# Kernel optimization log

Measured on AMD Instinct MI355X. Metric: run time of the kernel, lower is better.

Reference implementation:

```python
import jax, jax.numpy as jnp
import numpy as np
import math

CH = 512
HEADS = 8
GROUPS = 32
EPS = 1e-5


def group_norm(x, w, b):
    # x: [B, C, T]
    B, C, T = x.shape
    xg = x.reshape(B, GROUPS, C // GROUPS, T)
    mu = xg.mean(axis=(2, 3), keepdims=True)
    var = xg.var(axis=(2, 3), keepdims=True)
    xg = (xg - mu) * jax.lax.rsqrt(var + EPS)
    return xg.reshape(B, C, T) * w[None, :, None] + b[None, :, None]


def conv1x1(x, w, b):
    # x: [B, C, T], w: [O, C, 1]
    return jnp.einsum('oc,bct->bot', w[:, :, 0], x) + b[None, :, None]


def conv3_same(x, w, b):
    y = jax.lax.conv_general_dilated(x, w, window_strides=(1,), padding='SAME',
                                     dimension_numbers=('NCH', 'OIH', 'NCH'))
    return y + b[None, :, None]


def setup_inputs() -> dict:
    key = jax.random.key(0)
    ks = jax.random.split(key, 12)
    B, Ti, Ts = 2, 4096, 1024
    inp = {
        'image': jax.random.normal(ks[0], (B, Ti, CH), jnp.float32),
        'st': jax.random.normal(ks[1], (B, Ts, CH), jnp.float32),
        'xn_w': jnp.ones((CH,), jnp.float32),
        'xn_b': jnp.zeros((CH,), jnp.float32),
        'jn_w': jnp.ones((CH,), jnp.float32),
        'jn_b': jnp.zeros((CH,), jnp.float32),
        'xqkv_w': jax.random.normal(ks[2], (3 * CH, CH, 1), jnp.float32) * (1.0 / math.sqrt(CH)),
        'xqkv_b': jnp.zeros((3 * CH,), jnp.float32),
        'jqkv_w': jax.random.normal(ks[3], (3 * CH, CH, 1), jnp.float32) * (1.0 / math.sqrt(CH)),
        'jqkv_b': jnp.zeros((3 * CH,), jnp.float32),
        # NOTE: original zero-inits proj; we use small random weights so the
        # attention path contributes to the output (same math).
        'proj_w': jax.random.normal(ks[4], (CH, CH, 3), jnp.float32) * (0.02 / math.sqrt(3 * CH)),
        'proj_b': jnp.zeros((CH,), jnp.float32),
    }
    return inp


def reference(image, st, xn_w, xn_b, jn_w, jn_b, xqkv_w, xqkv_b, jqkv_w, jqkv_b, proj_w, proj_b):
    # image: [B, Ti, C]  st: [B, Ts, C]
    x = image.transpose(0, 2, 1)           # [B, C, Ti]
    jc = st.transpose(0, 2, 1)              # [B, C, Ts]

    x_qkv = conv1x1(group_norm(x, xn_w, xn_b), xqkv_w, xqkv_b)    # [B, 3C, Ti]
    jc_qkv = conv1x1(group_norm(jc, jn_w, jn_b), jqkv_w, jqkv_b)  # [B, 3C, Ts]

    B, _, Ti = x_qkv.shape
    ch = CH // HEADS
    scale = 1.0 / math.sqrt(math.sqrt(ch))

    img_q = x_qkv[:, :CH].reshape(B, HEADS, ch, Ti)
    st_k = jc_qkv[:, CH:2 * CH].reshape(B, HEADS, ch, -1)
    st_v = jc_qkv[:, 2 * CH:].reshape(B, HEADS, ch, -1)

    # cross-attention: image queries attend to st keys/values
    w = jnp.einsum('bhct,bhcs->bhts', img_q * scale, st_k * scale)  # [B,H,Ti,Ts]
    w = jax.nn.softmax(w.astype(jnp.float32), axis=-1).astype(w.dtype)
    attn = jnp.einsum('bhts,bhcs->bhct', w, st_v).reshape(B, CH, Ti)

    x_h = conv3_same(attn, proj_w, proj_b)
    return x + x_h  # [B, C, Ti]
```

## Files before the change

kernel.cpp:

```cpp
#include <hip/hip_runtime.h>
#include <math.h>

static constexpr int CH = 512;
static constexpr int GROUPS = 32;
static constexpr int HC = 64;
static constexpr float EPS = 1e-5f;
static constexpr int TI = 4096;
static constexpr int TS = 1024;

typedef __bf16 bf16x8 __attribute__((ext_vector_type(8)));
typedef __bf16 bf16x4 __attribute__((ext_vector_type(4)));
typedef float f32x4 __attribute__((ext_vector_type(4)));

__global__ __launch_bounds__(256) void k_gn_stats(const float* __restrict__ X, int T,
                                                  float* __restrict__ stats) {
  int b = blockIdx.x >> 5;
  int g = blockIdx.x & 31;
  int tid = threadIdx.x;
  const float* base = X + ((size_t)b * T) * CH + g * 16;
  double s1 = 0.0, s2 = 0.0;
  for (int t = tid; t < T; t += 256) {
    const float4* p = (const float4*)(base + (size_t)t * CH);
#pragma unroll
    for (int q = 0; q < 4; ++q) {
      float4 v = p[q];
      s1 += (double)v.x + (double)v.y + (double)v.z + (double)v.w;
      s2 += (double)v.x * v.x + (double)v.y * v.y + (double)v.z * v.z + (double)v.w * v.w;
    }
  }
  __shared__ double r1[256];
  __shared__ double r2[256];
  r1[tid] = s1;
  r2[tid] = s2;
  __syncthreads();
  for (int s = 128; s > 0; s >>= 1) {
    if (tid < s) { r1[tid] += r1[tid + s]; r2[tid] += r2[tid + s]; }
    __syncthreads();
  }
  if (tid == 0) {
    double N = (double)16 * T;
    double mu = r1[0] / N;
    double var = r2[0] / N - mu * mu;
    float rs = (float)(1.0 / sqrt(var + (double)EPS));
    stats[(b * GROUPS + g) * 2 + 0] = (float)mu;
    stats[(b * GROUPS + g) * 2 + 1] = rs;
  }
}

__global__ __launch_bounds__(256) void k_gn_apply(const float* __restrict__ X,
                                                  const float* __restrict__ stats,
                                                  const float* __restrict__ nw,
                                                  const float* __restrict__ nb,
                                                  __bf16* __restrict__ Xp, int T) {
  size_t idx = ((size_t)blockIdx.x * 256 + threadIdx.x) * 8;
  int b = (int)(idx / ((size_t)T * 512));
  size_t rem = idx - (size_t)b * T * 512;
  int t = (int)(rem >> 9);
  int c = (int)(rem & 511);
  int g = c >> 4;
  float mu = stats[(b * GROUPS + g) * 2 + 0];
  float rs = stats[(b * GROUPS + g) * 2 + 1];
  float4 v0 = *(const float4*)(X + idx);
  float4 v1 = *(const float4*)(X + idx + 4);
  float4 w0 = *(const float4*)(nw + c);
  float4 w1 = *(const float4*)(nw + c + 4);
  float4 q0 = *(const float4*)(nb + c);
  float4 q1 = *(const float4*)(nb + c + 4);
  float xv[8] = {v0.x, v0.y, v0.z, v0.w, v1.x, v1.y, v1.z, v1.w};
  float wv[8] = {w0.x, w0.y, w0.z, w0.w, w1.x, w1.y, w1.z, w1.w};
  float qv[8] = {q0.x, q0.y, q0.z, q0.w, q1.x, q1.y, q1.z, q1.w};
  bf16x8 r;
#pragma unroll
  for (int i = 0; i < 8; ++i) {
    float a = rs * wv[i];
    r[i] = (__bf16)fmaf(xv[i], a, qv[i] - mu * a);
  }
  size_t off = ((((size_t)b * (T >> 4) + (t >> 4)) * 16 + (c >> 5)) * 64 +
                ((c >> 3) & 3) * 16 + (t & 15)) * 8;
  *(bf16x8*)(Xp + off) = r;
}

__global__ __launch_bounds__(256) void k_wpack(const float* __restrict__ W,
                                               __bf16* __restrict__ Wp) {
  int idx = blockIdx.x * 256 + threadIdx.x;
  int lane = idx & 63;
  int l = lane & 15, g = lane >> 4;
  int cb = (idx >> 6) & 15;
  int ob = idx >> 10;
  const float* src = W + (size_t)(ob * 16 + l) * 512 + cb * 32 + g * 8;
  float4 v0 = *(const float4*)src;
  float4 v1 = *(const float4*)(src + 4);
  float xv[8] = {v0.x, v0.y, v0.z, v0.w, v1.x, v1.y, v1.z, v1.w};
  bf16x8 r;
#pragma unroll
  for (int i = 0; i < 8; ++i) r[i] = (__bf16)xv[i];
  *(bf16x8*)(Wp + (size_t)idx * 8) = r;
}

__global__ __launch_bounds__(256) void k_wpack3(const float* __restrict__ W,
                                                __bf16* __restrict__ W3p) {
  int idx = blockIdx.x * 256 + threadIdx.x;
  int lane = idx & 63;
  int l = lane & 15, g = lane >> 4;
  int ob = (idx >> 6) & 31;
  int q = idx >> 11;
  int tap = q % 3;
  int cb = q / 3;
  int o = ob * 16 + l;
  int c = cb * 32 + g * 8;
  bf16x8 r;
#pragma unroll
  for (int j = 0; j < 8; ++j) r[j] = (__bf16)W[((size_t)o * 512 + c + j) * 3 + tap];
  *(bf16x8*)(W3p + (size_t)idx * 8) = r;
}

__global__ __launch_bounds__(256) void k_qkv_mfma(const __bf16* __restrict__ Xp,
                                                  const __bf16* __restrict__ Wp,
                                                  const float* __restrict__ bias,
                                                  __bf16* __restrict__ outQK,
                                                  __bf16* __restrict__ outVp,
                                                  int T) {
  int b = blockIdx.z;
  int o0 = blockIdx.y * 64;
  int tid = threadIdx.x;
  int w = tid >> 6;
  int lane = tid & 63;
  int l = lane & 15;
  int g = lane >> 4;
  int t0 = blockIdx.x * 128 + w * 32;
  int Tb = T >> 4;
  bool vmode = (outVp != nullptr) && (o0 >= 512);

  __shared__ __align__(16) __bf16 Elds[4][2048];

  f32x4 acc[2][4] = {};
  const __bf16* Xb = Xp + (size_t)b * T * 512;

  auto load_c = [&](int cb, bf16x8 (&af)[2], bf16x8 (&wf)[4]) {
#pragma unroll
    for (int m = 0; m < 2; ++m)
      af[m] = *(const bf16x8*)(Xb + ((((size_t)(t0 >> 4) + m) * 16 + cb) * 64 + lane) * 8);
#pragma unroll
    for (int n = 0; n < 4; ++n)
      wf[n] = *(const bf16x8*)(Wp + ((((size_t)(o0 >> 4) + n) * 16 + cb) * 64 + lane) * 8);
  };

  bf16x8 afA[2], wfA[4], afB[2], wfB[4];
#define QKV_LOOP(MMEXPR)                                                        \
  {                                                                             \
    load_c(0, afA, wfA);                                                        \
    _Pragma("unroll") for (int cb = 0; cb < 16; cb += 2) {                      \
      load_c(cb + 1, afB, wfB);                                                 \
      _Pragma("unroll") for (int m = 0; m < 2; ++m)                             \
          _Pragma("unroll") for (int n = 0; n < 4; ++n) {                       \
        bf16x8 af = afA[m], wf = wfA[n];                                        \
        acc[m][n] = MMEXPR;                                                     \
      }                                                                         \
      if (cb + 2 < 16) load_c(cb + 2, afA, wfA);                                \
      _Pragma("unroll") for (int m = 0; m < 2; ++m)                             \
          _Pragma("unroll") for (int n = 0; n < 4; ++n) {                       \
        bf16x8 af = afB[m], wf = wfB[n];                                        \
        acc[m][n] = MMEXPR;                                                     \
      }                                                                         \
    }                                                                           \
  }

  if (!vmode) {
    QKV_LOOP(__builtin_amdgcn_mfma_f32_16x16x32_bf16(wf, af, acc[m][n], 0, 0, 0))
    float sc = (outVp == nullptr) ? 0.125f : 1.0f;
    int swz = (l & 7) << 1;
    __bf16(*Eq)[64] = reinterpret_cast<__bf16(*)[64]>(&Elds[w][0]);
#pragma unroll
    for (int m = 0; m < 2; ++m)
#pragma unroll
      for (int n = 0; n < 4; ++n) {
        f32x4 bv = *(const f32x4*)(bias + o0 + 16 * n + 4 * g);
        bf16x4 pv;
#pragma unroll
        for (int r = 0; r < 4; ++r) pv[r] = (__bf16)((acc[m][n][r] + bv[r]) * sc);
        *(bf16x4*)&Eq[m * 16 + l][((4 * n + g) ^ swz) * 4] = pv;
      }
#pragma unroll
    for (int m = 0; m < 2; ++m)
#pragma unroll
      for (int cbi = 0; cbi < 2; ++cbi) {
        bf16x8 v = *(const bf16x8*)&Eq[m * 16 + l][((8 * cbi + 2 * g) ^ swz) * 4];
        *(bf16x8*)(outQK +
                   ((((size_t)b * Tb + (t0 >> 4) + m) * 16 + (o0 >> 5) + cbi) * 64 + lane) * 8) = v;
      }
  } else {
    QKV_LOOP(__builtin_amdgcn_mfma_f32_16x16x32_bf16(af, wf, acc[m][n], 0, 0, 0))
    int swzv = l & 6;
    __bf16(*Ev)[32] = reinterpret_cast<__bf16(*)[32]>(&Elds[w][0]);
#pragma unroll
    for (int m = 0; m < 2; ++m)
#pragma unroll
      for (int n = 0; n < 4; ++n) {
        float bo = bias[o0 + 16 * n + l];
        bf16x4 pv;
#pragma unroll
        for (int r = 0; r < 4; ++r) pv[r] = (__bf16)(acc[m][n][r] + bo);
        *(bf16x4*)&Ev[16 * n + l][((4 * m + g) ^ swzv) * 4] = pv;
      }
#pragma unroll
    for (int n = 0; n < 4; ++n) {
      bf16x8 v = *(const bf16x8*)&Ev[16 * n + l][((2 * g) ^ swzv) * 4];
      int cb16 = ((o0 - 512) >> 4) + n;
      *(bf16x8*)(outVp + ((((size_t)b * 32 + cb16) * 32 + (t0 >> 5)) * 64 + lane) * 8) = v;
    }
  }
#undef QKV_LOOP
}

__global__ __launch_bounds__(128, 4) void k_attn_mfma(const __bf16* __restrict__ Qp,
                                                      const __bf16* __restrict__ Kp,
                                                      const __bf16* __restrict__ Vp,
                                                      __bf16* __restrict__ outA) {
  int b = blockIdx.z;
  int h = blockIdx.y;
  int tid = threadIdx.x;
  int w = tid >> 6;
  int lane = tid & 63;
  int l = lane & 15;
  int g = lane >> 4;
  int t0 = blockIdx.x * 32;
  int swz = (l & 7) << 1;

  __shared__ __align__(16) __bf16 Pt[2][2][16][64];
  __shared__ float Ored[64][32];
  __shared__ float Lred[64][2];

  bf16x8 qf[2][2];
#pragma unroll
  for (int m = 0; m < 2; ++m)
#pragma unroll
    for (int ks = 0; ks < 2; ++ks)
      qf[m][ks] = *(const bf16x8*)(Qp + ((((size_t)b * 256 + (t0 >> 4) + m) * 16 +
                                          2 * h + ks) * 64 + lane) * 8);

  f32x4 o_acc[2][4] = {};
  float rs_acc[2] = {};

  int s_base = w * 512;
#pragma unroll 1
  for (int s0 = s_base; s0 < s_base + 512; s0 += 64) {
    bf16x8 kf[4][2];
#pragma unroll
    for (int n = 0; n < 4; ++n)
#pragma unroll
      for (int ks = 0; ks < 2; ++ks)
        kf[n][ks] = *(const bf16x8*)(Kp + ((((size_t)b * 64 + (s0 >> 4) + n) * 16 +
                                            2 * h + ks) * 64 + lane) * 8);
    bf16x8 vf[4][2];
#pragma unroll
    for (int n = 0; n < 4; ++n)
#pragma unroll
      for (int ks = 0; ks < 2; ++ks)
        vf[n][ks] = *(const bf16x8*)(Vp + ((((size_t)b * 32 + h * 4 + n) * 32 +
                                            (s0 >> 5) + ks) * 64 + lane) * 8);
    f32x4 sT[4][2];
#pragma unroll
    for (int sb = 0; sb < 4; ++sb)
#pragma unroll
      for (int tb = 0; tb < 2; ++tb) {
        f32x4 z = {0.f, 0.f, 0.f, 0.f};
        z = __builtin_amdgcn_mfma_f32_16x16x32_bf16(kf[sb][0], qf[tb][0], z, 0, 0, 0);
        sT[sb][tb] = __builtin_amdgcn_mfma_f32_16x16x32_bf16(kf[sb][1], qf[tb][1], z, 0, 0, 0);
      }
#pragma unroll
    for (int tb = 0; tb < 2; ++tb)
#pragma unroll
      for (int sb = 0; sb < 4; ++sb) {
        float p0 = __expf(sT[sb][tb][0]);
        float p1 = __expf(sT[sb][tb][1]);
        float p2 = __expf(sT[sb][tb][2]);
        float p3 = __expf(sT[sb][tb][3]);
        rs_acc[tb] += (p0 + p1) + (p2 + p3);
        bf16x4 pv;
        pv[0] = (__bf16)p0;
        pv[1] = (__bf16)p1;
        pv[2] = (__bf16)p2;
        pv[3] = (__bf16)p3;
        *(bf16x4*)&Pt[w][tb][l][((4 * sb + g) ^ swz) * 4] = pv;
      }
    bf16x8 pa[2][2];
#pragma unroll
    for (int tb = 0; tb < 2; ++tb)
#pragma unroll
      for (int ks = 0; ks < 2; ++ks)
        pa[tb][ks] = *(const bf16x8*)&Pt[w][tb][l][((8 * ks + 2 * g) ^ swz) * 4];
#pragma unroll
    for (int tb = 0; tb < 2; ++tb)
#pragma unroll
      for (int n = 0; n < 4; ++n) {
        o_acc[tb][n] = __builtin_amdgcn_mfma_f32_16x16x32_bf16(vf[n][0], pa[tb][0], o_acc[tb][n], 0, 0, 0);
        o_acc[tb][n] = __builtin_amdgcn_mfma_f32_16x16x32_bf16(vf[n][1], pa[tb][1], o_acc[tb][n], 0, 0, 0);
      }
  }

  if (w == 1) {
#pragma unroll
    for (int tb = 0; tb < 2; ++tb) {
#pragma unroll
      for (int n = 0; n < 4; ++n)
#pragma unroll
        for (int r = 0; r < 4; ++r) Ored[lane][tb * 16 + n * 4 + r] = o_acc[tb][n][r];
      Lred[lane][tb] = rs_acc[tb];
    }
  }
  __syncthreads();
  if (w == 0) {
#pragma unroll
    for (int tb = 0; tb < 2; ++tb) {
#pragma unroll
      for (int n = 0; n < 4; ++n)
#pragma unroll
        for (int r = 0; r < 4; ++r) o_acc[tb][n][r] += Ored[lane][tb * 16 + n * 4 + r];
      float v = rs_acc[tb] + Lred[lane][tb];
      v += __shfl_xor(v, 16, 64);
      v += __shfl_xor(v, 32, 64);
      float inv = 1.f / v;
#pragma unroll
      for (int n = 0; n < 4; ++n) {
        bf16x4 ov;
#pragma unroll
        for (int r = 0; r < 4; ++r) ov[r] = (__bf16)(o_acc[tb][n][r] * inv);
        *(bf16x4*)(outA + ((size_t)b * TI + t0 + 16 * tb + l) * 512 + h * 64 + 16 * n + 4 * g) = ov;
      }
    }
  }
}

__global__ __launch_bounds__(256) void k_conv3_mfma(const __bf16* __restrict__ A,
                                                    const __bf16* __restrict__ W3p,
                                                    const float* __restrict__ bias,
                                                    const float* __restrict__ image,
                                                    float* __restrict__ out) {
  int b = blockIdx.z;
  int o0 = blockIdx.y * 64;
  int ob0 = o0 >> 4;
  int tid = threadIdx.x;
  int w = tid >> 6;
  int lane = tid & 63;
  int l = lane & 15;
  int g = lane >> 4;
  int t0 = blockIdx.x * 128;
  int t0w = t0 + w * 32;

  __shared__ __align__(16) __bf16 Alds[2][130 * 32];
  __shared__ __align__(16) __bf16 Wlds[2][12 * 512];

  const __bf16* Ab = A + (size_t)b * TI * 512;

  auto stage = [&](int cb, int buf) {
#pragma unroll
    for (int pass = 0; pass < 3; ++pass) {
      int gi = tid + pass * 256;
      if (gi < 520) {
        int r = gi >> 2, gg = gi & 3;
        int t = t0 - 1 + r;
        bf16x8 v = {};
        if (t >= 0 && t < TI) v = *(const bf16x8*)(Ab + (size_t)t * 512 + cb * 32 + gg * 8);
        *(bf16x8*)&Alds[buf][r * 32 + ((gg ^ (r & 3)) << 3)] = v;
      }
    }
#pragma unroll
    for (int ch = w; ch < 12; ch += 4) {
      bf16x8 v = *(const bf16x8*)(W3p + ((((size_t)cb * 3 + (ch >> 2)) * 32 + ob0 +
                                          (ch & 3)) * 64 + lane) * 8);
      *(bf16x8*)&Wlds[buf][ch * 512 + lane * 8] = v;
    }
  };

  f32x4 acc[2][4] = {};

  stage(0, 0);
  __syncthreads();
#pragma unroll 1
  for (int cs = 0; cs < 16; ++cs) {
    int cur = cs & 1;
    if (cs < 15) stage(cs + 1, cur ^ 1);
    bf16x8 af[3][2], wf[3][4];
#pragma unroll
    for (int tap = 0; tap < 3; ++tap) {
#pragma unroll
      for (int m = 0; m < 2; ++m) {
        int r = w * 32 + 16 * m + l + tap;
        af[tap][m] = *(const bf16x8*)&Alds[cur][r * 32 + ((g ^ (r & 3)) << 3)];
      }
#pragma unroll
      for (int n = 0; n < 4; ++n)
        wf[tap][n] = *(const bf16x8*)&Wlds[cur][(tap * 4 + n) * 512 + lane * 8];
    }
#pragma unroll
    for (int tap = 0; tap < 3; ++tap)
#pragma unroll
      for (int m = 0; m < 2; ++m)
#pragma unroll
        for (int n = 0; n < 4; ++n)
          acc[m][n] =
              __builtin_amdgcn_mfma_f32_16x16x32_bf16(af[tap][m], wf[tap][n], acc[m][n], 0, 0, 0);
    __syncthreads();
  }

#pragma unroll
  for (int m = 0; m < 2; ++m) {
    int tb = t0w + 16 * m + 4 * g;
#pragma unroll
    for (int n = 0; n < 4; ++n) {
      int o = o0 + 16 * n + l;
      float bo = bias[o];
      f32x4 r;
#pragma unroll
      for (int rr = 0; rr < 4; ++rr)
        r[rr] = acc[m][n][rr] + bo + image[((size_t)b * TI + tb + rr) * CH + o];
      *(f32x4*)(out + ((size_t)b * CH + o) * TI + tb) = r;
    }
  }
}

extern "C" void kernel_launch(void* const* d_in, const int* in_sizes, int n_in,
                              void* d_out, int out_size, void* d_ws, size_t ws_size,
                              hipStream_t stream) {
  const float* image = (const float*)d_in[0];
  const float* st = (const float*)d_in[1];
  const float* xn_w = (const float*)d_in[2];
  const float* xn_b = (const float*)d_in[3];
  const float* jn_w = (const float*)d_in[4];
  const float* jn_b = (const float*)d_in[5];
  const float* xqkv_w = (const float*)d_in[6];
  const float* xqkv_b = (const float*)d_in[7];
  const float* jqkv_w = (const float*)d_in[8];
  const float* jqkv_b = (const float*)d_in[9];
  const float* proj_w = (const float*)d_in[10];
  const float* proj_b = (const float*)d_in[11];
  float* out = (float*)d_out;
  float* ws = (float*)d_ws;

  float* stats_x = ws;
  float* stats_j = ws + 128;
  __bf16* Xnp = (__bf16*)(ws + 256);
  __bf16* abuf = Xnp;
  __bf16* stnp = Xnp + (size_t)2 * TI * CH;
  __bf16* wqb = stnp + (size_t)2 * TS * CH;
  __bf16* wkvb = wqb + (size_t)CH * CH;
  __bf16* wb3 = wkvb + (size_t)2 * CH * CH;
  __bf16* Qp = wb3 + (size_t)3 * CH * CH;
  __bf16* Kp = Qp + (size_t)2 * TI * CH;
  __bf16* Vp = Kp + (size_t)2 * TS * CH;

  k_gn_stats<<<dim3(64), dim3(256), 0, stream>>>(image, TI, stats_x);
  k_gn_stats<<<dim3(64), dim3(256), 0, stream>>>(st, TS, stats_j);

  k_gn_apply<<<dim3(2 * TI * 512 / 2048), dim3(256), 0, stream>>>(image, stats_x, xn_w, xn_b, Xnp, TI);
  k_gn_apply<<<dim3(2 * TS * 512 / 2048), dim3(256), 0, stream>>>(st, stats_j, jn_w, jn_b, stnp, TS);

  k_wpack<<<dim3(128), dim3(256), 0, stream>>>(xqkv_w, wqb);
  k_wpack<<<dim3(256), dim3(256), 0, stream>>>(jqkv_w + (size_t)CH * CH, wkvb);
  k_wpack3<<<dim3(384), dim3(256), 0, stream>>>(proj_w, wb3);

  k_qkv_mfma<<<dim3(TI / 128, CH / 64, 2), dim3(256), 0, stream>>>(
      Xnp, wqb, xqkv_b, Qp, nullptr, TI);
  k_qkv_mfma<<<dim3(TS / 128, 1024 / 64, 2), dim3(256), 0, stream>>>(
      stnp, wkvb, jqkv_b + CH, Kp, Vp, TS);

  k_attn_mfma<<<dim3(TI / 32, 8, 2), dim3(128), 0, stream>>>(Qp, Kp, Vp, abuf);

  k_conv3_mfma<<<dim3(TI / 128, CH / 64, 2), dim3(256), 0, stream>>>(
      abuf, wb3, proj_b, image, out);
}
```

Baseline: 123.7 us.

## Split group-norm stats across chunks, merge small launches, fold log2e into Q scale

The group-norm statistics pass now splits each (batch, group) over 8 time chunks and processes both inputs in one grid of 1024 blocks, followed by a tiny finalize kernel. Before, only 64 blocks per input handled these reductions serially. The two norm-apply launches and the three weight-pack launches are each merged into a single kernel to cut launch count. The Q scale also absorbs log2(e), so the attention softmax can use exp2f instead of __expf.

```diff
diff --git a/kernel.cpp b/kernel.cpp
--- a/kernel.cpp
+++ b/kernel.cpp
@@ -12,14 +12,22 @@
 typedef __bf16 bf16x4 __attribute__((ext_vector_type(4)));
 typedef float f32x4 __attribute__((ext_vector_type(4)));
 
-__global__ __launch_bounds__(256) void k_gn_stats(const float* __restrict__ X, int T,
-                                                  float* __restrict__ stats) {
-  int b = blockIdx.x >> 5;
-  int g = blockIdx.x & 31;
+__global__ __launch_bounds__(256) void k_gn_partial(const float* __restrict__ img,
+                                                    const float* __restrict__ st,
+                                                    double* __restrict__ part) {
+  int bi = blockIdx.x;
+  int which = bi >> 9;
+  int rem = bi & 511;
+  int b = rem >> 8;
+  int g = (rem >> 3) & 31;
+  int chunk = rem & 7;
+  const float* X = which ? st : img;
+  int T = which ? TS : TI;
+  int rows = T >> 3;
   int tid = threadIdx.x;
-  const float* base = X + ((size_t)b * T) * CH + g * 16;
+  const float* base = X + ((size_t)b * T + (size_t)chunk * rows) * CH + g * 16;
   double s1 = 0.0, s2 = 0.0;
-  for (int t = tid; t < T; t += 256) {
+  for (int t = tid; t < rows; t += 256) {
     const float4* p = (const float4*)(base + (size_t)t * CH);
 #pragma unroll
     for (int q = 0; q < 4; ++q) {
@@ -38,21 +46,54 @@
     __syncthreads();
   }
   if (tid == 0) {
-    double N = (double)16 * T;
-    double mu = r1[0] / N;
-    double var = r2[0] / N - mu * mu;
-    float rs = (float)(1.0 / sqrt(var + (double)EPS));
-    stats[(b * GROUPS + g) * 2 + 0] = (float)mu;
-    stats[(b * GROUPS + g) * 2 + 1] = rs;
-  }
-}
-
-__global__ __launch_bounds__(256) void k_gn_apply(const float* __restrict__ X,
-                                                  const float* __restrict__ stats,
-                                                  const float* __restrict__ nw,
-                                                  const float* __restrict__ nb,
-                                                  __bf16* __restrict__ Xp, int T) {
-  size_t idx = ((size_t)blockIdx.x * 256 + threadIdx.x) * 8;
+    part[bi * 2 + 0] = r1[0];
+    part[bi * 2 + 1] = r2[0];
+  }
+}
+
+__global__ __launch_bounds__(128) void k_gn_final(const double* __restrict__ part,
+                                                  float* __restrict__ stats_x,
+                                                  float* __restrict__ stats_j) {
+  int tid = threadIdx.x;
+  int which = tid >> 6;
+  int idx = tid & 63;
+  const double* p = part + ((which << 9) + ((idx >> 5) << 8) + ((idx & 31) << 3)) * 2;
+  double s1 = 0.0, s2 = 0.0;
+#pragma unroll
+  for (int c = 0; c < 8; ++c) {
+    s1 += p[c * 2 + 0];
+    s2 += p[c * 2 + 1];
+  }
+  int T = which ? TS : TI;
+  double N = 16.0 * T;
+  double mu = s1 / N;
+  double var = s2 / N - mu * mu;
+  float rs = (float)(1.0 / sqrt(var + (double)EPS));
+  float* stats = which ? stats_j : stats_x;
+  stats[idx * 2 + 0] = (float)mu;
+  stats[idx * 2 + 1] = rs;
+}
+
+__global__ __launch_bounds__(256) void k_gn_apply2(const float* __restrict__ img,
+                                                   const float* __restrict__ st,
+                                                   const float* __restrict__ stats_x,
+                                                   const float* __restrict__ stats_j,
+                                                   const float* __restrict__ xn_w,
+                                                   const float* __restrict__ xn_b,
+                                                   const float* __restrict__ jn_w,
+                                                   const float* __restrict__ jn_b,
+                                                   __bf16* __restrict__ Xnp,
+                                                   __bf16* __restrict__ stnp) {
+  int bi = blockIdx.x;
+  bool isimg = bi < 2048;
+  const float* X = isimg ? img : st;
+  const float* stats = isimg ? stats_x : stats_j;
+  const float* nw = isimg ? xn_w : jn_w;
+  const float* nb = isimg ? xn_b : jn_b;
+  __bf16* Xp = isimg ? Xnp : stnp;
+  int T = isimg ? TI : TS;
+  size_t idx = ((size_t)(isimg ? bi : bi - 2048) * 256 + threadIdx.x) * 8;
+
   int b = (int)(idx / ((size_t)T * 512));
   size_t rem = idx - (size_t)b * T * 512;
   int t = (int)(rem >> 9);
@@ -80,38 +121,44 @@
   *(bf16x8*)(Xp + off) = r;
 }
 
-__global__ __launch_bounds__(256) void k_wpack(const float* __restrict__ W,
-                                               __bf16* __restrict__ Wp) {
-  int idx = blockIdx.x * 256 + threadIdx.x;
-  int lane = idx & 63;
-  int l = lane & 15, g = lane >> 4;
-  int cb = (idx >> 6) & 15;
-  int ob = idx >> 10;
-  const float* src = W + (size_t)(ob * 16 + l) * 512 + cb * 32 + g * 8;
-  float4 v0 = *(const float4*)src;
-  float4 v1 = *(const float4*)(src + 4);
-  float xv[8] = {v0.x, v0.y, v0.z, v0.w, v1.x, v1.y, v1.z, v1.w};
-  bf16x8 r;
-#pragma unroll
-  for (int i = 0; i < 8; ++i) r[i] = (__bf16)xv[i];
-  *(bf16x8*)(Wp + (size_t)idx * 8) = r;
-}
-
-__global__ __launch_bounds__(256) void k_wpack3(const float* __restrict__ W,
-                                                __bf16* __restrict__ W3p) {
-  int idx = blockIdx.x * 256 + threadIdx.x;
-  int lane = idx & 63;
-  int l = lane & 15, g = lane >> 4;
-  int ob = (idx >> 6) & 31;
-  int q = idx >> 11;
-  int tap = q % 3;
-  int cb = q / 3;
-  int o = ob * 16 + l;
-  int c = cb * 32 + g * 8;
-  bf16x8 r;
-#pragma unroll
-  for (int j = 0; j < 8; ++j) r[j] = (__bf16)W[((size_t)o * 512 + c + j) * 3 + tap];
-  *(bf16x8*)(W3p + (size_t)idx * 8) = r;
+__global__ __launch_bounds__(256) void k_pack_all(const float* __restrict__ xqkv_w,
+                                                  const float* __restrict__ jqkv_w,
+                                                  const float* __restrict__ proj_w,
+                                                  __bf16* __restrict__ wqb,
+                                                  __bf16* __restrict__ wkvb,
+                                                  __bf16* __restrict__ wb3) {
+  int bi = blockIdx.x;
+  if (bi < 384) {
+    const float* W = (bi < 128) ? xqkv_w : (jqkv_w + (size_t)CH * CH);
+    __bf16* Wp = (bi < 128) ? wqb : wkvb;
+    int idx = ((bi < 128) ? bi : bi - 128) * 256 + threadIdx.x;
+    int lane = idx & 63;
+    int l = lane & 15, g = lane >> 4;
+    int cb = (idx >> 6) & 15;
+    int ob = idx >> 10;
+    const float* src = W + (size_t)(ob * 16 + l) * 512 + cb * 32 + g * 8;
+    float4 v0 = *(const float4*)src;
+    float4 v1 = *(const float4*)(src + 4);
+    float xv[8] = {v0.x, v0.y, v0.z, v0.w, v1.x, v1.y, v1.z, v1.w};
+    bf16x8 r;
+#pragma unroll
+    for (int i = 0; i < 8; ++i) r[i] = (__bf16)xv[i];
+    *(bf16x8*)(Wp + (size_t)idx * 8) = r;
+  } else {
+    int idx = (bi - 384) * 256 + threadIdx.x;
+    int lane = idx & 63;
+    int l = lane & 15, g = lane >> 4;
+    int ob = (idx >> 6) & 31;
+    int q = idx >> 11;
+    int tap = q % 3;
+    int cb = q / 3;
+    int o = ob * 16 + l;
+    int c = cb * 32 + g * 8;
+    bf16x8 r;
+#pragma unroll
+    for (int j = 0; j < 8; ++j) r[j] = (__bf16)proj_w[((size_t)o * 512 + c + j) * 3 + tap];
+    *(bf16x8*)(wb3 + (size_t)idx * 8) = r;
+  }
 }
 
 __global__ __launch_bounds__(256) void k_qkv_mfma(const __bf16* __restrict__ Xp,
@@ -167,7 +214,7 @@
 
   if (!vmode) {
     QKV_LOOP(__builtin_amdgcn_mfma_f32_16x16x32_bf16(wf, af, acc[m][n], 0, 0, 0))
-    float sc = (outVp == nullptr) ? 0.125f : 1.0f;
+    float sc = (outVp == nullptr) ? 0.125f * 1.44269504088896f : 1.0f;
     int swz = (l & 7) << 1;
     __bf16(*Eq)[64] = reinterpret_cast<__bf16(*)[64]>(&Elds[w][0]);
 #pragma unroll
@@ -271,10 +318,10 @@
     for (int tb = 0; tb < 2; ++tb)
 #pragma unroll
       for (int sb = 0; sb < 4; ++sb) {
-        float p0 = __expf(sT[sb][tb][0]);
-        float p1 = __expf(sT[sb][tb][1]);
-        float p2 = __expf(sT[sb][tb][2]);
-        float p3 = __expf(sT[sb][tb][3]);
+        float p0 = exp2f(sT[sb][tb][0]);
+        float p1 = exp2f(sT[sb][tb][1]);
+        float p2 = exp2f(sT[sb][tb][2]);
+        float p3 = exp2f(sT[sb][tb][3]);
         rs_acc[tb] += (p0 + p1) + (p2 + p3);
         bf16x4 pv;
         pv[0] = (__bf16)p0;
@@ -437,9 +484,10 @@
   float* out = (float*)d_out;
   float* ws = (float*)d_ws;
 
-  float* stats_x = ws;
-  float* stats_j = ws + 128;
-  __bf16* Xnp = (__bf16*)(ws + 256);
+  double* part = (double*)ws;
+  float* stats_x = ws + 4096;
+  float* stats_j = ws + 4096 + 128;
+  __bf16* Xnp = (__bf16*)(ws + 4096 + 256);
   __bf16* abuf = Xnp;
   __bf16* stnp = Xnp + (size_t)2 * TI * CH;
   __bf16* wqb = stnp + (size_t)2 * TS * CH;
@@ -449,15 +497,13 @@
   __bf16* Kp = Qp + (size_t)2 * TI * CH;
   __bf16* Vp = Kp + (size_t)2 * TS * CH;
 
-  k_gn_stats<<<dim3(64), dim3(256), 0, stream>>>(image, TI, stats_x);
-  k_gn_stats<<<dim3(64), dim3(256), 0, stream>>>(st, TS, stats_j);
-
-  k_gn_apply<<<dim3(2 * TI * 512 / 2048), dim3(256), 0, stream>>>(image, stats_x, xn_w, xn_b, Xnp, TI);
-  k_gn_apply<<<dim3(2 * TS * 512 / 2048), dim3(256), 0, stream>>>(st, stats_j, jn_w, jn_b, stnp, TS);
-
-  k_wpack<<<dim3(128), dim3(256), 0, stream>>>(xqkv_w, wqb);
-  k_wpack<<<dim3(256), dim3(256), 0, stream>>>(jqkv_w + (size_t)CH * CH, wkvb);
-  k_wpack3<<<dim3(384), dim3(256), 0, stream>>>(proj_w, wb3);
+  k_gn_partial<<<dim3(1024), dim3(256), 0, stream>>>(image, st, part);
+  k_gn_final<<<dim3(1), dim3(128), 0, stream>>>(part, stats_x, stats_j);
+
+  k_gn_apply2<<<dim3(2560), dim3(256), 0, stream>>>(image, st, stats_x, stats_j,
+                                                    xn_w, xn_b, jn_w, jn_b, Xnp, stnp);
+
+  k_pack_all<<<dim3(768), dim3(256), 0, stream>>>(xqkv_w, jqkv_w, proj_w, wqb, wkvb, wb3);
 
   k_qkv_mfma<<<dim3(TI / 128, CH / 64, 2), dim3(256), 0, stream>>>(
       Xnp, wqb, xqkv_b, Qp, nullptr, TI);
```

Measured after the change: 117.2 us. 5.3% less time.
